# Kernel optimization log

Hardware: AMD Instinct MI355X
Metric: run time of the kernel (lower is better)

Reference implementation:

```python
import jax, jax.numpy as jnp
import numpy as np

B, L, D, H, MD = 8, 1024, 1024, 16, 6
DF = 4 * D
HD = D // H
EPS = 1e-5


def setup_inputs() -> dict:
    key = jax.random.key(0)
    ks = jax.random.split(key, 12)
    s = 0.02
    n = lambda k, shape: jax.random.normal(k, shape, dtype=jnp.float32) * s
    return {
        "x": jax.random.normal(ks[0], (B, L, D), dtype=jnp.float32),
        # attention sub-block
        "attn_norm_w": jnp.ones((D,), jnp.float32),
        "attn_norm_b": jnp.zeros((D,), jnp.float32),
        "in_proj_w": n(ks[1], (3 * D, D)),
        "in_proj_b": jnp.zeros((3 * D,), jnp.float32),
        "out_proj_w": n(ks[2], (D, D)),
        "out_proj_b": jnp.zeros((D,), jnp.float32),
        # ffn sub-block
        "ffn_norm_w": jnp.ones((D,), jnp.float32),
        "ffn_norm_b": jnp.zeros((D,), jnp.float32),
        "ffn_w1": n(ks[3], (DF, D)),
        "ffn_b1": jnp.zeros((DF,), jnp.float32),
        "ffn_w2": n(ks[4], (D, DF)),
        "ffn_b2": jnp.zeros((D,), jnp.float32),
        # router
        "rt_norm_w": jnp.ones((D,), jnp.float32),
        "rt_norm_b": jnp.zeros((D,), jnp.float32),
        "rt_w1": n(ks[5], (D, D)),
        "rt_b1": jnp.zeros((D,), jnp.float32),
        "rt_w2": n(ks[6], (MD, D)),
        "rt_b2": jnp.zeros((MD,), jnp.float32),
    }


def _layernorm(x, w, b):
    mu = jnp.mean(x, axis=-1, keepdims=True)
    var = jnp.mean(jnp.square(x - mu), axis=-1, keepdims=True)
    return (x - mu) * jax.lax.rsqrt(var + EPS) * w + b


def _mha(x, in_proj_w, in_proj_b, out_proj_w, out_proj_b):
    # packed qkv projection, torch nn.MultiheadAttention semantics (batch_first)
    qkv = x @ in_proj_w.T + in_proj_b                      # (B,L,3D)
    q, k, v = jnp.split(qkv, 3, axis=-1)
    def heads(t):
        return t.reshape(B, L, H, HD).transpose(0, 2, 1, 3)  # (B,H,L,HD)
    q, k, v = heads(q), heads(k), heads(v)
    scores = jnp.einsum("bhqd,bhkd->bhqk", q, k) / jnp.sqrt(jnp.float32(HD))
    attn = jax.nn.softmax(scores, axis=-1)
    ctx = jnp.einsum("bhqk,bhkd->bhqd", attn, v)           # (B,H,L,HD)
    ctx = ctx.transpose(0, 2, 1, 3).reshape(B, L, D)
    return ctx @ out_proj_w.T + out_proj_b


def _block(x, p):
    # pre-norm attention + residual
    a_in = _layernorm(x, p["attn_norm_w"], p["attn_norm_b"])
    x = x + _mha(a_in, p["in_proj_w"], p["in_proj_b"], p["out_proj_w"], p["out_proj_b"])
    # pre-norm FFN + residual (exact erf GELU, matching torch nn.GELU default)
    f_in = _layernorm(x, p["ffn_norm_w"], p["ffn_norm_b"])
    h = jax.nn.gelu(f_in @ p["ffn_w1"].T + p["ffn_b1"], approximate=False)
    x = x + h @ p["ffn_w2"].T + p["ffn_b2"]
    return x


def reference(x, attn_norm_w, attn_norm_b, in_proj_w, in_proj_b, out_proj_w,
              out_proj_b, ffn_norm_w, ffn_norm_b, ffn_w1, ffn_b1, ffn_w2,
              ffn_b2, rt_norm_w, rt_norm_b, rt_w1, rt_b1, rt_w2, rt_b2):
    p = dict(attn_norm_w=attn_norm_w, attn_norm_b=attn_norm_b,
             in_proj_w=in_proj_w, in_proj_b=in_proj_b,
             out_proj_w=out_proj_w, out_proj_b=out_proj_b,
             ffn_norm_w=ffn_norm_w, ffn_norm_b=ffn_norm_b,
             ffn_w1=ffn_w1, ffn_b1=ffn_b1, ffn_w2=ffn_w2, ffn_b2=ffn_b2)
    # router (eval mode: argmax, no Gumbel noise)
    r_in = _layernorm(x, rt_norm_w, rt_norm_b)
    h = jax.nn.gelu(r_in @ rt_w1.T + rt_b1, approximate=False)
    logits = h @ rt_w2.T + rt_b2                           # (B,L,MD)
    depths = jnp.argmax(logits, axis=-1) + 1               # (B,L) in [1,MD]
    cur = x
    for level in range(1, MD + 1):
        upd = _block(cur, p)
        cont = (depths >= level)[..., None]
        cur = jnp.where(cont, upd, cur)
    return cur, depths, logits
```

## Files before the change

kernel.cpp:

```cpp
#include <hip/hip_runtime.h>
#include <cstdint>
#include <cstddef>

typedef __bf16 bf16;
typedef bf16 bf16x8 __attribute__((ext_vector_type(8)));
typedef float f32x4 __attribute__((ext_vector_type(4)));

#define GAS __attribute__((address_space(1)))
#define LAS __attribute__((address_space(3)))

__device__ __forceinline__ void async_cp16(const bf16* g, bf16* l) {
  __builtin_amdgcn_global_load_lds((const GAS unsigned int*)g,
                                   (LAS unsigned int*)l, 16, 0, 0);
}

__device__ __forceinline__ float gelu_f(float x) {
  return 0.5f * x * (1.0f + erff(x * 0.70710678118654752440f));
}

__global__ void __launch_bounds__(256) f2b_kernel(const float* __restrict__ in,
                                                  bf16* __restrict__ out, int n) {
  int i = (blockIdx.x * 256 + threadIdx.x) * 4;
  if (i >= n) return;
  float4 v = *(const float4*)&in[i];
  union { uint2 u; bf16 e[4]; } o;
  o.e[0] = (bf16)v.x; o.e[1] = (bf16)v.y; o.e[2] = (bf16)v.z; o.e[3] = (bf16)v.w;
  *(uint2*)&out[i] = o.u;
}

__global__ void __launch_bounds__(256) split3_kernel(const float* __restrict__ in,
    bf16* __restrict__ oh, bf16* __restrict__ om, bf16* __restrict__ ol, int n) {
  int i = (blockIdx.x * 256 + threadIdx.x) * 4;
  if (i >= n) return;
  float4 v = *(const float4*)&in[i];
  float a[4] = {v.x, v.y, v.z, v.w};
  union { uint2 u; bf16 e[4]; } h, m, l;
#pragma unroll
  for (int j = 0; j < 4; j++) {
    h.e[j] = (bf16)a[j];
    float r = a[j] - (float)h.e[j];
    m.e[j] = (bf16)r;
    l.e[j] = (bf16)(r - (float)m.e[j]);
  }
  *(uint2*)&oh[i] = h.u;
  *(uint2*)&om[i] = m.u;
  *(uint2*)&ol[i] = l.u;
}

template<int SPLIT>
__global__ void __launch_bounds__(256) ln_kernel(const float* __restrict__ X,
    const float* __restrict__ w, const float* __restrict__ b,
    bf16* __restrict__ oh, bf16* __restrict__ om, bf16* __restrict__ ol) {
  const int row = blockIdx.x;
  const int tid = threadIdx.x;
  const float4 xv = *(const float4*)&X[(size_t)row * 1024 + tid * 4];
  float s1 = xv.x + xv.y + xv.z + xv.w;
  float s2 = xv.x * xv.x + xv.y * xv.y + xv.z * xv.z + xv.w * xv.w;
#pragma unroll
  for (int d = 1; d < 64; d <<= 1) {
    s1 += __shfl_xor(s1, d, 64);
    s2 += __shfl_xor(s2, d, 64);
  }
  __shared__ float red[8];
  if ((tid & 63) == 0) { red[tid >> 6] = s1; red[4 + (tid >> 6)] = s2; }
  __syncthreads();
  s1 = red[0] + red[1] + red[2] + red[3];
  s2 = red[4] + red[5] + red[6] + red[7];
  const float mu = s1 * (1.0f / 1024.0f);
  const float var = s2 * (1.0f / 1024.0f) - mu * mu;
  const float rs = rsqrtf(var + 1e-5f);
  const float4 wv = *(const float4*)&w[tid * 4];
  const float4 bv = *(const float4*)&b[tid * 4];
  float y[4] = {(xv.x - mu) * rs * wv.x + bv.x,
                (xv.y - mu) * rs * wv.y + bv.y,
                (xv.z - mu) * rs * wv.z + bv.z,
                (xv.w - mu) * rs * wv.w + bv.w};
  union { uint2 u; bf16 e[4]; } h;
#pragma unroll
  for (int j = 0; j < 4; j++) h.e[j] = (bf16)y[j];
  *(uint2*)&oh[(size_t)row * 1024 + tid * 4] = h.u;
  if (SPLIT == 3) {
    union { uint2 u; bf16 e[4]; } m, l;
#pragma unroll
    for (int j = 0; j < 4; j++) {
      float r = y[j] - (float)h.e[j];
      m.e[j] = (bf16)r;
      l.e[j] = (bf16)(r - (float)m.e[j]);
    }
    *(uint2*)&om[(size_t)row * 1024 + tid * 4] = m.u;
    *(uint2*)&ol[(size_t)row * 1024 + tid * 4] = l.u;
  }
}

__device__ __forceinline__ void swizzle_mn(int gx, int& m0, int& n0) {
  const int id = blockIdx.y * gx + blockIdx.x;
  const int k8 = id & 7, t = id >> 3;
  n0 = (t % gx) * 128;
  m0 = ((t / gx) * 8 + k8) * 128;
}

template<int MODE>
__global__ void __launch_bounds__(256) gemm_nt(
    const bf16* __restrict__ A, const bf16* __restrict__ B,
    const float* __restrict__ bias, const float* __restrict__ Res,
    float* __restrict__ C32, bf16* __restrict__ Cb,
    const int* __restrict__ gate, int M, int N, int K, int level) {
  __shared__ bf16 As[128 * 32];
  __shared__ bf16 Bs[128 * 32];
  const int tid = threadIdx.x;
  const int w = tid >> 6, lane = tid & 63;
  const int lr = lane & 15, lq = lane >> 4;
  int m0, n0;
  swizzle_mn(gridDim.x, m0, n0);
  const int wm = (w >> 1) * 64, wn = (w & 1) * 64;

  f32x4 acc[4][4] = {};

  const bf16* ga = A + (size_t)(m0 + (tid >> 2)) * K + (tid & 3) * 8;
  const bf16* gb = B + (size_t)(n0 + (tid >> 2)) * K + (tid & 3) * 8;
  bf16* la = As + w * 512;
  bf16* lb = Bs + w * 512;
  const size_t step64 = (size_t)64 * K;

  for (int k0 = 0; k0 < K; k0 += 32) {
    __syncthreads();
    async_cp16(ga + k0, la);
    async_cp16(ga + step64 + k0, la + 2048);
    async_cp16(gb + k0, lb);
    async_cp16(gb + step64 + k0, lb + 2048);
    __syncthreads();
    bf16x8 af[4], bfr[4];
#pragma unroll
    for (int i = 0; i < 4; i++)
      af[i] = *(const bf16x8*)&As[(wm + i * 16 + lr) * 32 + lq * 8];
#pragma unroll
    for (int i = 0; i < 4; i++)
      bfr[i] = *(const bf16x8*)&Bs[(wn + i * 16 + lr) * 32 + lq * 8];
#pragma unroll
    for (int mi = 0; mi < 4; mi++)
#pragma unroll
      for (int ni = 0; ni < 4; ni++)
        acc[mi][ni] = __builtin_amdgcn_mfma_f32_16x16x32_bf16(
            af[mi], bfr[ni], acc[mi][ni], 0, 0, 0);
  }

#pragma unroll
  for (int mi = 0; mi < 4; mi++) {
    const int rbase = m0 + wm + mi * 16 + lq * 4;
#pragma unroll
    for (int ni = 0; ni < 4; ni++) {
      const int c = n0 + wn + ni * 16 + lr;
      float bv = 0.0f;
      if (MODE <= 3) bv = bias[c];
#pragma unroll
      for (int r = 0; r < 4; r++) {
        const size_t row = (size_t)(rbase + r);
        const float v = acc[mi][ni][r];
        if (MODE == 0) {
          Cb[row * N + c] = (bf16)(v + bv);
        } else if (MODE == 1) {
          C32[row * N + c] = Res[row * N + c] + v + bv;
        } else if (MODE == 2) {
          Cb[row * N + c] = (bf16)gelu_f(v + bv);
        } else if (MODE == 3) {
          if (gate[row] >= level) C32[row * N + c] = Res[row * N + c] + v + bv;
        } else if (MODE == 4) {
          C32[row * N + c] += v;
        } else {
          C32[row * N + c] = v;
        }
      }
    }
  }
}

__global__ void __launch_bounds__(256) gemm_router(
    const bf16* __restrict__ Ah, const bf16* __restrict__ Am, const bf16* __restrict__ Al,
    const bf16* __restrict__ Bh, const bf16* __restrict__ Bm, const bf16* __restrict__ Bl,
    float* __restrict__ C32) {
  __shared__ bf16 As[3][128 * 32];
  __shared__ bf16 Bs[3][128 * 32];
  const int tid = threadIdx.x;
  const int w = tid >> 6, lane = tid & 63;
  const int lr = lane & 15, lq = lane >> 4;
  int m0, n0;
  swizzle_mn(gridDim.x, m0, n0);
  const int wm = (w >> 1) * 64, wn = (w & 1) * 64;
  const int K = 1024;

  f32x4 acc[4][4] = {};

  const size_t aoff = (size_t)(m0 + (tid >> 2)) * K + (tid & 3) * 8;
  const size_t boff = (size_t)(n0 + (tid >> 2)) * K + (tid & 3) * 8;
  const bf16* gA[3] = {Ah + aoff, Am + aoff, Al + aoff};
  const bf16* gB[3] = {Bh + boff, Bm + boff, Bl + boff};
  const int lo = w * 512;
  const size_t step64 = (size_t)64 * K;

  const int cA[6] = {0, 0, 1, 1, 0, 2};
  const int cB[6] = {0, 1, 0, 1, 2, 0};

  for (int k0 = 0; k0 < K; k0 += 32) {
    __syncthreads();
#pragma unroll
    for (int j = 0; j < 3; j++) {
      async_cp16(gA[j] + k0, As[j] + lo);
      async_cp16(gA[j] + step64 + k0, As[j] + lo + 2048);
      async_cp16(gB[j] + k0, Bs[j] + lo);
      async_cp16(gB[j] + step64 + k0, Bs[j] + lo + 2048);
    }
    __syncthreads();
#pragma unroll
    for (int c = 0; c < 6; c++) {
      bf16x8 af[4], bfr[4];
#pragma unroll
      for (int i = 0; i < 4; i++)
        af[i] = *(const bf16x8*)&As[cA[c]][(wm + i * 16 + lr) * 32 + lq * 8];
#pragma unroll
      for (int i = 0; i < 4; i++)
        bfr[i] = *(const bf16x8*)&Bs[cB[c]][(wn + i * 16 + lr) * 32 + lq * 8];
#pragma unroll
      for (int mi = 0; mi < 4; mi++)
#pragma unroll
        for (int ni = 0; ni < 4; ni++)
          acc[mi][ni] = __builtin_amdgcn_mfma_f32_16x16x32_bf16(
              af[mi], bfr[ni], acc[mi][ni], 0, 0, 0);
    }
  }

#pragma unroll
  for (int mi = 0; mi < 4; mi++) {
    const int rbase = m0 + wm + mi * 16 + lq * 4;
#pragma unroll
    for (int ni = 0; ni < 4; ni++) {
      const int c = n0 + wn + ni * 16 + lr;
#pragma unroll
      for (int r = 0; r < 4; r++)
        C32[(size_t)(rbase + r) * 1024 + c] = acc[mi][ni][r];
    }
  }
}

__global__ void __launch_bounds__(256) gelu_bias_kernel(float* __restrict__ t,
    const float* __restrict__ bias, int n) {
  int i = (blockIdx.x * 256 + threadIdx.x) * 4;
  if (i >= n) return;
  float4 v = *(const float4*)&t[i];
  float4 bb = *(const float4*)&bias[i & 1023];
  v.x = gelu_f(v.x + bb.x);
  v.y = gelu_f(v.y + bb.y);
  v.z = gelu_f(v.z + bb.z);
  v.w = gelu_f(v.w + bb.w);
  *(float4*)&t[i] = v;
}

__global__ void __launch_bounds__(256) router_logits(const float* __restrict__ h,
    const float* __restrict__ w2, const float* __restrict__ b2,
    float* __restrict__ logits_out, float* __restrict__ depths_out,
    int* __restrict__ gate) {
  const int row = blockIdx.x * 4 + (threadIdx.x >> 6);
  const int lane = threadIdx.x & 63;
  const float* hr = h + (size_t)row * 1024;
  float part[6] = {0, 0, 0, 0, 0, 0};
  for (int kc = lane; kc < 256; kc += 64) {
    float4 hv = *(const float4*)&hr[kc * 4];
#pragma unroll
    for (int j = 0; j < 6; j++) {
      float4 wv = *(const float4*)&w2[j * 1024 + kc * 4];
      part[j] += hv.x * wv.x + hv.y * wv.y + hv.z * wv.z + hv.w * wv.w;
    }
  }
#pragma unroll
  for (int j = 0; j < 6; j++)
#pragma unroll
    for (int d = 1; d < 64; d <<= 1) part[j] += __shfl_xor(part[j], d, 64);
  if (lane == 0) {
    float best = -1e30f;
    int bi = 0;
#pragma unroll
    for (int j = 0; j < 6; j++) {
      const float v = part[j] + b2[j];
      logits_out[(size_t)row * 6 + j] = v;
      if (v > best) { best = v; bi = j; }
    }
    depths_out[row] = (float)(bi + 1);
    gate[row] = bi + 1;
  }
}

__global__ void __launch_bounds__(256) vtrans_kernel(const bf16* __restrict__ qkv,
                                                     bf16* __restrict__ vt) {
  __shared__ bf16 T[64 * 64];
  const int tid = threadIdx.x;
  const int tb = blockIdx.x & 15, bh = blockIdx.x >> 4;
  const int b = bh >> 4, h = bh & 15;
#pragma unroll
  for (int i = 0; i < 2; i++) {
    const int c = tid + i * 256;
    const int tok = c >> 3, hd8 = (c & 7) * 8;
    uint4 v = *(const uint4*)&qkv[((size_t)b * 1024 + tb * 64 + tok) * 3072 + 2048 + h * 64 + hd8];
    *(uint4*)&T[tok * 64 + (hd8 ^ ((tok & 7) << 3))] = v;
  }
  __syncthreads();
#pragma unroll
  for (int i = 0; i < 2; i++) {
    const int c = tid + i * 256;
    const int hd = c >> 3, t8 = (c & 7) * 8;
    union { uint4 u; bf16 e[8]; } o;
#pragma unroll
    for (int j = 0; j < 8; j++)
      o.e[j] = T[(t8 + j) * 64 + (hd ^ (j << 3))];
    *(uint4*)&vt[((size_t)bh * 64 + hd) * 1024 + tb * 64 + t8] = o.u;
  }
}

__global__ void __launch_bounds__(256) attn_kernel(const bf16* __restrict__ qkv,
                                                   const bf16* __restrict__ vtg,
                                                   bf16* __restrict__ ctx) {
  __shared__ bf16 Qs[64 * 72];
  __shared__ bf16 Ks[64 * 72];
  __shared__ bf16 Vt[64 * 72];
  __shared__ bf16 Ps[64 * 72];
  const int tid = threadIdx.x;
  const int w = tid >> 6, lane = tid & 63;
  const int lr = lane & 15, lq = lane >> 4;
  const int blk = blockIdx.x;
  const int bh = (blk & 7) | ((blk >> 7) << 3);
  const int qt = (blk >> 3) & 15;
  const int b = bh >> 4, h = bh & 15;
  const size_t rowbase = (size_t)b * 1024;
  const int hcol = h * 64;
  const size_t vbase = (size_t)bh * 65536;

#pragma unroll
  for (int i = 0; i < 2; i++) {
    const int c = tid + i * 256;
    const int r = c >> 3, k8 = (c & 7) * 8;
    uint4 v = *(const uint4*)&qkv[(rowbase + qt * 64 + r) * 3072 + hcol + k8];
    *(uint4*)&Qs[r * 72 + k8] = v;
  }
  __syncthreads();
  bf16x8 aq[2];
#pragma unroll
  for (int hs = 0; hs < 2; hs++)
    aq[hs] = *(const bf16x8*)&Qs[(w * 16 + lr) * 72 + hs * 32 + lq * 8];

  float lsum[4] = {0.0f, 0.0f, 0.0f, 0.0f};
  f32x4 o[4];
#pragma unroll
  for (int i = 0; i < 4; i++) o[i] = (f32x4)0.0f;

  const int Sw = ((w * 4 + lq) & 7) << 3;
  const int Sr = ((w * 4 + (lr >> 2)) & 7) << 3;

  for (int kb = 0; kb < 16; kb++) {
    __syncthreads();
#pragma unroll
    for (int i = 0; i < 2; i++) {
      const int c = tid + i * 256;
      const int r = c >> 3, k8 = (c & 7) * 8;
      uint4 v = *(const uint4*)&qkv[(rowbase + kb * 64 + r) * 3072 + 1024 + hcol + k8];
      *(uint4*)&Ks[r * 72 + k8] = v;
    }
#pragma unroll
    for (int i = 0; i < 2; i++) {
      const int c = tid + i * 256;
      const int hd = c >> 3, t8 = (c & 7) * 8;
      uint4 v = *(const uint4*)&vtg[vbase + (size_t)hd * 1024 + kb * 64 + t8];
      *(uint4*)&Vt[hd * 72 + (t8 ^ (hd & 56))] = v;
    }
    __syncthreads();

    f32x4 s[4];
#pragma unroll
    for (int kf = 0; kf < 4; kf++) {
      f32x4 sa = (f32x4)0.0f;
#pragma unroll
      for (int hs = 0; hs < 2; hs++) {
        bf16x8 bk = *(const bf16x8*)&Ks[(kf * 16 + lr) * 72 + hs * 32 + lq * 8];
        sa = __builtin_amdgcn_mfma_f32_16x16x32_bf16(aq[hs], bk, sa, 0, 0, 0);
      }
      s[kf] = sa;
    }

#pragma unroll
    for (int kf = 0; kf < 4; kf++) {
#pragma unroll
      for (int r = 0; r < 4; r++) {
        const float p = __expf(s[kf][r] * 0.125f);
        lsum[r] += p;
        const int row = w * 16 + lq * 4 + r;
        Ps[row * 72 + ((kf * 16 + lr) ^ Sw)] = (bf16)p;
      }
    }

    bf16x8 ap[2];
#pragma unroll
    for (int ks = 0; ks < 2; ks++)
      ap[ks] = *(const bf16x8*)&Ps[(w * 16 + lr) * 72 + ((ks * 32 + lq * 8) ^ Sr)];
#pragma unroll
    for (int hf = 0; hf < 4; hf++) {
      const int vrow = hf * 16 + lr;
#pragma unroll
      for (int ks = 0; ks < 2; ks++) {
        bf16x8 bv = *(const bf16x8*)&Vt[vrow * 72 + ((ks * 32 + lq * 8) ^ (vrow & 56))];
        o[hf] = __builtin_amdgcn_mfma_f32_16x16x32_bf16(ap[ks], bv, o[hf], 0, 0, 0);
      }
    }
  }

#pragma unroll
  for (int r = 0; r < 4; r++) {
#pragma unroll
    for (int d = 1; d < 16; d <<= 1) lsum[r] += __shfl_xor(lsum[r], d, 64);
  }

#pragma unroll
  for (int r = 0; r < 4; r++) {
    const float inv = 1.0f / lsum[r];
    const size_t row = rowbase + qt * 64 + w * 16 + lq * 4 + r;
#pragma unroll
    for (int hf = 0; hf < 4; hf++)
      ctx[row * 1024 + hcol + hf * 16 + lr] = (bf16)(o[hf][r] * inv);
  }
}

extern "C" void kernel_launch(void* const* d_in, const int* in_sizes, int n_in,
                              void* d_out, int out_size, void* d_ws, size_t ws_size,
                              hipStream_t stream) {
  (void)in_sizes; (void)n_in; (void)out_size; (void)ws_size;
  const float* x    = (const float*)d_in[0];
  const float* a_nw = (const float*)d_in[1];
  const float* a_nb = (const float*)d_in[2];
  const float* in_w = (const float*)d_in[3];
  const float* in_b = (const float*)d_in[4];
  const float* o_w  = (const float*)d_in[5];
  const float* o_b  = (const float*)d_in[6];
  const float* f_nw = (const float*)d_in[7];
  const float* f_nb = (const float*)d_in[8];
  const float* w1   = (const float*)d_in[9];
  const float* b1   = (const float*)d_in[10];
  const float* w2   = (const float*)d_in[11];
  const float* b2   = (const float*)d_in[12];
  const float* r_nw = (const float*)d_in[13];
  const float* r_nb = (const float*)d_in[14];
  const float* rw1  = (const float*)d_in[15];
  const float* rb1  = (const float*)d_in[16];
  const float* rw2  = (const float*)d_in[17];
  const float* rb2  = (const float*)d_in[18];

  float* cur    = (float*)d_out;
  float* depths = cur + 8388608;
  float* logits = depths + 8192;

  char* ws = (char*)d_ws;
  bf16* wb_in  = (bf16*)(ws + 0);
  bf16* wb_out = (bf16*)(ws + 6291456);
  bf16* wb_f1  = (bf16*)(ws + 8388608);
  bf16* wb_f2  = (bf16*)(ws + 16777216);
  bf16* r1h    = (bf16*)(ws + 25165824);
  bf16* r1m    = (bf16*)(ws + 27262976);
  bf16* r1l    = (bf16*)(ws + 29360128);
  bf16* Abuf   = (bf16*)(ws + 31457280);
  bf16* Bbuf   = (bf16*)(ws + 48234496);
  bf16* Big    = (bf16*)(ws + 65011712);
  float* Tmp   = (float*)(ws + 132120576);
  bf16* VtG    = (bf16*)(ws + 132120576);
  int*  gate   = (int*)(ws + 165675008);

  hipMemcpyAsync(cur, x, (size_t)8388608 * 4, hipMemcpyDeviceToDevice, stream);

  f2b_kernel<<<3072, 256, 0, stream>>>(in_w, wb_in, 3145728);
  f2b_kernel<<<1024, 256, 0, stream>>>(o_w, wb_out, 1048576);
  f2b_kernel<<<4096, 256, 0, stream>>>(w1, wb_f1, 4194304);
  f2b_kernel<<<4096, 256, 0, stream>>>(w2, wb_f2, 4194304);
  split3_kernel<<<1024, 256, 0, stream>>>(rw1, r1h, r1m, r1l, 1048576);

  ln_kernel<3><<<8192, 256, 0, stream>>>(x, r_nw, r_nb, Abuf, Bbuf, Big);
  gemm_router<<<dim3(8, 64), 256, 0, stream>>>(Abuf, Bbuf, Big, r1h, r1m, r1l, Tmp);
  gelu_bias_kernel<<<8192, 256, 0, stream>>>(Tmp, rb1, 8388608);
  router_logits<<<2048, 256, 0, stream>>>(Tmp, rw2, rb2, logits, depths, gate);

  for (int level = 1; level <= 6; level++) {
    ln_kernel<1><<<8192, 256, 0, stream>>>(cur, a_nw, a_nb, Abuf, nullptr, nullptr);
    gemm_nt<0><<<dim3(24, 64), 256, 0, stream>>>(Abuf, wb_in, in_b, nullptr, nullptr, Big, nullptr, 8192, 3072, 1024, 0);
    vtrans_kernel<<<2048, 256, 0, stream>>>(Big, VtG);
    attn_kernel<<<2048, 256, 0, stream>>>(Big, VtG, Bbuf);
    gemm_nt<1><<<dim3(8, 64), 256, 0, stream>>>(Bbuf, wb_out, o_b, cur, Tmp, nullptr, nullptr, 8192, 1024, 1024, 0);
    ln_kernel<1><<<8192, 256, 0, stream>>>(Tmp, f_nw, f_nb, Abuf, nullptr, nullptr);
    gemm_nt<2><<<dim3(32, 64), 256, 0, stream>>>(Abuf, wb_f1, b1, nullptr, nullptr, Big, nullptr, 8192, 4096, 1024, 0);
    gemm_nt<3><<<dim3(8, 64), 256, 0, stream>>>(Big, wb_f2, b2, Tmp, cur, nullptr, gate, 8192, 1024, 4096, level);
  }
}
```

Measured before the change: 2.820 ms.

## Compact active tokens per depth level and skip work for halted rows

Builds per-level index lists of the tokens whose routed depth reaches that level. Only those rows are processed by the Q projection, attention queries, out-projection, FFN layernorm and both FFN GEMMs; K/V are still computed for all tokens. Blocks whose tile lies beyond the active count exit early, which removes the work wasted on rows that would be discarded by the gate. The cost is gathered row loads, index lookups in the epilogues, and a small atomic-based index build whose token order is nondeterministic.

```diff
diff --git a/kernel.cpp b/kernel.cpp
--- a/kernel.cpp
+++ b/kernel.cpp
@@ -92,6 +92,69 @@
   }
 }
 
+__global__ void __launch_bounds__(256) ln_c_kernel(const float* __restrict__ X,
+    const float* __restrict__ w, const float* __restrict__ b,
+    bf16* __restrict__ oh, const int* __restrict__ cnt_ptr) {
+  const int row = blockIdx.x;
+  const int cnt = *cnt_ptr;
+  const int pad = (cnt + 127) & ~127;
+  if (row >= pad) return;
+  const int tid = threadIdx.x;
+  if (row >= cnt) {
+    *(uint2*)&oh[(size_t)row * 1024 + tid * 4] = make_uint2(0, 0);
+    return;
+  }
+  const float4 xv = *(const float4*)&X[(size_t)row * 1024 + tid * 4];
+  float s1 = xv.x + xv.y + xv.z + xv.w;
+  float s2 = xv.x * xv.x + xv.y * xv.y + xv.z * xv.z + xv.w * xv.w;
+#pragma unroll
+  for (int d = 1; d < 64; d <<= 1) {
+    s1 += __shfl_xor(s1, d, 64);
+    s2 += __shfl_xor(s2, d, 64);
+  }
+  __shared__ float red[8];
+  if ((tid & 63) == 0) { red[tid >> 6] = s1; red[4 + (tid >> 6)] = s2; }
+  __syncthreads();
+  s1 = red[0] + red[1] + red[2] + red[3];
+  s2 = red[4] + red[5] + red[6] + red[7];
+  const float mu = s1 * (1.0f / 1024.0f);
+  const float var = s2 * (1.0f / 1024.0f) - mu * mu;
+  const float rs = rsqrtf(var + 1e-5f);
+  const float4 wv = *(const float4*)&w[tid * 4];
+  const float4 bv = *(const float4*)&b[tid * 4];
+  union { uint2 u; bf16 e[4]; } h;
+  h.e[0] = (bf16)((xv.x - mu) * rs * wv.x + bv.x);
+  h.e[1] = (bf16)((xv.y - mu) * rs * wv.y + bv.y);
+  h.e[2] = (bf16)((xv.z - mu) * rs * wv.z + bv.z);
+  h.e[3] = (bf16)((xv.w - mu) * rs * wv.w + bv.w);
+  *(uint2*)&oh[(size_t)row * 1024 + tid * 4] = h.u;
+}
+
+__global__ void zero_cnt_kernel(int* cnt_all, int* bcnt_all) {
+  if (threadIdx.x < 6) cnt_all[threadIdx.x] = 0;
+  if (threadIdx.x < 48) bcnt_all[threadIdx.x] = 0;
+}
+
+__global__ void __launch_bounds__(256) build_idx_kernel(
+    const int* __restrict__ gate, int* __restrict__ idx_all,
+    int* __restrict__ cnt_all, int* __restrict__ bidx_all,
+    int* __restrict__ bcnt_all) {
+  const int lev = blockIdx.x >> 3;
+  const int b   = blockIdx.x & 7;
+  const int level = lev + 1;
+  int* idx  = idx_all + lev * 8192;
+  int* bidx = bidx_all + lev * 8192 + b * 1024;
+  for (int t = threadIdx.x; t < 1024; t += 256) {
+    const int row = b * 1024 + t;
+    if (gate[row] >= level) {
+      int p = atomicAdd(&bcnt_all[lev * 8 + b], 1);
+      bidx[p] = t;
+      int q = atomicAdd(&cnt_all[lev], 1);
+      idx[q] = row;
+    }
+  }
+}
+
 __device__ __forceinline__ void swizzle_mn(int gx, int& m0, int& n0) {
   const int id = blockIdx.y * gx + blockIdx.x;
   const int k8 = id & 7, t = id >> 3;
@@ -104,7 +167,8 @@
     const bf16* __restrict__ A, const bf16* __restrict__ B,
     const float* __restrict__ bias, const float* __restrict__ Res,
     float* __restrict__ C32, bf16* __restrict__ Cb,
-    const int* __restrict__ gate, int M, int N, int K, int level) {
+    const int* __restrict__ idx, const int* __restrict__ cnt_ptr,
+    int N, int K, int ldc, int coff) {
   __shared__ bf16 As[128 * 32];
   __shared__ bf16 Bs[128 * 32];
   const int tid = threadIdx.x;
@@ -112,22 +176,36 @@
   const int lr = lane & 15, lq = lane >> 4;
   int m0, n0;
   swizzle_mn(gridDim.x, m0, n0);
+  int cnt = 0x7fffffff;
+  if (MODE != 0) {
+    cnt = *cnt_ptr;
+    if (m0 >= cnt) return;
+  }
   const int wm = (w >> 1) * 64, wn = (w & 1) * 64;
 
   f32x4 acc[4][4] = {};
 
-  const bf16* ga = A + (size_t)(m0 + (tid >> 2)) * K + (tid & 3) * 8;
+  const int i0 = m0 + (tid >> 2), i1 = i0 + 64;
+  size_t ar0, ar1;
+  if (MODE == 1 || MODE == 2) {
+    ar0 = (size_t)idx[i0 < cnt ? i0 : 0];
+    ar1 = (size_t)idx[i1 < cnt ? i1 : 0];
+  } else {
+    ar0 = (size_t)i0; ar1 = (size_t)i1;
+  }
+  const bf16* ga0 = A + ar0 * K + (tid & 3) * 8;
+  const bf16* ga1 = A + ar1 * K + (tid & 3) * 8;
   const bf16* gb = B + (size_t)(n0 + (tid >> 2)) * K + (tid & 3) * 8;
   bf16* la = As + w * 512;
   bf16* lb = Bs + w * 512;
-  const size_t step64 = (size_t)64 * K;
+  const size_t bstep = (size_t)64 * K;
 
   for (int k0 = 0; k0 < K; k0 += 32) {
     __syncthreads();
-    async_cp16(ga + k0, la);
-    async_cp16(ga + step64 + k0, la + 2048);
+    async_cp16(ga0 + k0, la);
+    async_cp16(ga1 + k0, la + 2048);
     async_cp16(gb + k0, lb);
-    async_cp16(gb + step64 + k0, lb + 2048);
+    async_cp16(gb + bstep + k0, lb + 2048);
     __syncthreads();
     bf16x8 af[4], bfr[4];
 #pragma unroll
@@ -147,27 +225,33 @@
 #pragma unroll
   for (int mi = 0; mi < 4; mi++) {
     const int rbase = m0 + wm + mi * 16 + lq * 4;
+    int orig[4];
+#pragma unroll
+    for (int r = 0; r < 4; r++) {
+      const int i = rbase + r;
+      if (MODE == 1 || MODE == 2 || MODE == 4) orig[r] = (i < cnt) ? idx[i] : -1;
+      else orig[r] = i;
+    }
 #pragma unroll
     for (int ni = 0; ni < 4; ni++) {
       const int c = n0 + wn + ni * 16 + lr;
-      float bv = 0.0f;
-      if (MODE <= 3) bv = bias[c];
+      const float bv = bias[c];
 #pragma unroll
       for (int r = 0; r < 4; r++) {
-        const size_t row = (size_t)(rbase + r);
-        const float v = acc[mi][ni][r];
+        const float v = acc[mi][ni][r] + bv;
+        const int i = rbase + r;
         if (MODE == 0) {
-          Cb[row * N + c] = (bf16)(v + bv);
+          Cb[(size_t)i * ldc + coff + c] = (bf16)v;
         } else if (MODE == 1) {
-          C32[row * N + c] = Res[row * N + c] + v + bv;
+          if (orig[r] >= 0) Cb[(size_t)orig[r] * ldc + c] = (bf16)v;
         } else if (MODE == 2) {
-          Cb[row * N + c] = (bf16)gelu_f(v + bv);
+          const float rv = (orig[r] >= 0) ? Res[(size_t)orig[r] * N + c] : 0.0f;
+          C32[(size_t)i * N + c] = rv + v;
         } else if (MODE == 3) {
-          if (gate[row] >= level) C32[row * N + c] = Res[row * N + c] + v + bv;
-        } else if (MODE == 4) {
-          C32[row * N + c] += v;
+          Cb[(size_t)i * N + c] = (bf16)gelu_f(v);
         } else {
-          C32[row * N + c] = v;
+          if (orig[r] >= 0)
+            C32[(size_t)orig[r] * N + c] = Res[(size_t)i * N + c] + v;
         }
       }
     }
@@ -315,12 +399,13 @@
 }
 
 __global__ void __launch_bounds__(256) attn_kernel(const bf16* __restrict__ qkv,
-                                                   const bf16* __restrict__ vtg,
-                                                   bf16* __restrict__ ctx) {
+    const bf16* __restrict__ vtg, bf16* __restrict__ ctx,
+    const int* __restrict__ bidx, const int* __restrict__ bcnt) {
   __shared__ bf16 Qs[64 * 72];
   __shared__ bf16 Ks[64 * 72];
   __shared__ bf16 Vt[64 * 72];
   __shared__ bf16 Ps[64 * 72];
+  __shared__ int Ts[64];
   const int tid = threadIdx.x;
   const int w = tid >> 6, lane = tid & 63;
   const int lr = lane & 15, lq = lane >> 4;
@@ -328,15 +413,23 @@
   const int bh = (blk & 7) | ((blk >> 7) << 3);
   const int qt = (blk >> 3) & 15;
   const int b = bh >> 4, h = bh & 15;
+  const int nb = bcnt[b];
+  if (qt * 64 >= nb) return;
   const size_t rowbase = (size_t)b * 1024;
   const int hcol = h * 64;
   const size_t vbase = (size_t)bh * 65536;
 
+  if (tid < 64) {
+    const int j = qt * 64 + tid;
+    Ts[tid] = (j < nb) ? bidx[b * 1024 + j] : bidx[b * 1024 + qt * 64];
+  }
+  __syncthreads();
+
 #pragma unroll
   for (int i = 0; i < 2; i++) {
     const int c = tid + i * 256;
     const int r = c >> 3, k8 = (c & 7) * 8;
-    uint4 v = *(const uint4*)&qkv[(rowbase + qt * 64 + r) * 3072 + hcol + k8];
+    uint4 v = *(const uint4*)&qkv[(rowbase + Ts[r]) * 3072 + hcol + k8];
     *(uint4*)&Qs[r * 72 + k8] = v;
   }
   __syncthreads();
@@ -417,11 +510,14 @@
 
 #pragma unroll
   for (int r = 0; r < 4; r++) {
-    const float inv = 1.0f / lsum[r];
-    const size_t row = rowbase + qt * 64 + w * 16 + lq * 4 + r;
-#pragma unroll
-    for (int hf = 0; hf < 4; hf++)
-      ctx[row * 1024 + hcol + hf * 16 + lr] = (bf16)(o[hf][r] * inv);
+    const int rowj = w * 16 + lq * 4 + r;
+    if (qt * 64 + rowj < nb) {
+      const float inv = 1.0f / lsum[r];
+      const size_t row = rowbase + Ts[rowj];
+#pragma unroll
+      for (int hf = 0; hf < 4; hf++)
+        ctx[row * 1024 + hcol + hf * 16 + lr] = (bf16)(o[hf][r] * inv);
+    }
   }
 }
 
@@ -467,6 +563,10 @@
   float* Tmp   = (float*)(ws + 132120576);
   bf16* VtG    = (bf16*)(ws + 132120576);
   int*  gate   = (int*)(ws + 165675008);
+  int* idx_all  = (int*)(ws + 25165824);
+  int* bidx_all = (int*)(ws + 27262976);
+  int* cnt_all  = (int*)(ws + 29360128);
+  int* bcnt_all = cnt_all + 16;
 
   hipMemcpyAsync(cur, x, (size_t)8388608 * 4, hipMemcpyDeviceToDevice, stream);
 
@@ -480,15 +580,29 @@
   gemm_router<<<dim3(8, 64), 256, 0, stream>>>(Abuf, Bbuf, Big, r1h, r1m, r1l, Tmp);
   gelu_bias_kernel<<<8192, 256, 0, stream>>>(Tmp, rb1, 8388608);
   router_logits<<<2048, 256, 0, stream>>>(Tmp, rw2, rb2, logits, depths, gate);
+  zero_cnt_kernel<<<1, 64, 0, stream>>>(cnt_all, bcnt_all);
+  build_idx_kernel<<<48, 256, 0, stream>>>(gate, idx_all, cnt_all, bidx_all, bcnt_all);
 
   for (int level = 1; level <= 6; level++) {
+    const int lev = level - 1;
+    const int* idxL  = idx_all + lev * 8192;
+    const int* cntL  = cnt_all + lev;
+    const int* bidxL = bidx_all + lev * 8192;
+    const int* bcntL = bcnt_all + lev * 8;
+
     ln_kernel<1><<<8192, 256, 0, stream>>>(cur, a_nw, a_nb, Abuf, nullptr, nullptr);
-    gemm_nt<0><<<dim3(24, 64), 256, 0, stream>>>(Abuf, wb_in, in_b, nullptr, nullptr, Big, nullptr, 8192, 3072, 1024, 0);
+    gemm_nt<0><<<dim3(16, 64), 256, 0, stream>>>(Abuf, wb_in + 1048576, in_b + 1024,
+        nullptr, nullptr, Big, nullptr, nullptr, 2048, 1024, 3072, 1024);
+    gemm_nt<1><<<dim3(8, 64), 256, 0, stream>>>(Abuf, wb_in, in_b,
+        nullptr, nullptr, Big, idxL, cntL, 1024, 1024, 3072, 0);
     vtrans_kernel<<<2048, 256, 0, stream>>>(Big, VtG);
-    attn_kernel<<<2048, 256, 0, stream>>>(Big, VtG, Bbuf);
-    gemm_nt<1><<<dim3(8, 64), 256, 0, stream>>>(Bbuf, wb_out, o_b, cur, Tmp, nullptr, nullptr, 8192, 1024, 1024, 0);
-    ln_kernel<1><<<8192, 256, 0, stream>>>(Tmp, f_nw, f_nb, Abuf, nullptr, nullptr);
-    gemm_nt<2><<<dim3(32, 64), 256, 0, stream>>>(Abuf, wb_f1, b1, nullptr, nullptr, Big, nullptr, 8192, 4096, 1024, 0);
-    gemm_nt<3><<<dim3(8, 64), 256, 0, stream>>>(Big, wb_f2, b2, Tmp, cur, nullptr, gate, 8192, 1024, 4096, level);
-  }
-}
+    attn_kernel<<<2048, 256, 0, stream>>>(Big, VtG, Bbuf, bidxL, bcntL);
+    gemm_nt<2><<<dim3(8, 64), 256, 0, stream>>>(Bbuf, wb_out, o_b,
+        cur, Tmp, nullptr, idxL, cntL, 1024, 1024, 0, 0);
+    ln_c_kernel<<<8192, 256, 0, stream>>>(Tmp, f_nw, f_nb, Abuf, cntL);
+    gemm_nt<3><<<dim3(32, 64), 256, 0, stream>>>(Abuf, wb_f1, b1,
+        nullptr, nullptr, Big, idxL, cntL, 4096, 1024, 0, 0);
+    gemm_nt<4><<<dim3(8, 64), 256, 0, stream>>>(Big, wb_f2, b2,
+        Tmp, cur, nullptr, idxL, cntL, 1024, 4096, 0, 0);
+  }
+}
```

Result: faster. 2.586 ms (-8.3%).
